# Performance work log

Measured on AMD Instinct MI355X. Metric: run time of the kernel, lower is better.

## Reference

```python
import jax, jax.numpy as jnp
import numpy as np

D_MODEL = 512
N_HEADS = 8
D_KV = 64
EPS = 1e-6
ROPE_THETA = 10000.0


def _rms_norm(x, w):
    # T5-style RMSNorm: no mean subtraction, no bias, variance in fp32.
    var = jnp.mean(x.astype(jnp.float32) ** 2, axis=-1, keepdims=True)
    return (x * jax.lax.rsqrt(var + EPS)).astype(x.dtype) * w


def _rope_cos_sin(pos, dk):
    # pos: [B, T] int -> cos/sin: [B, 1, T, dk]
    inv_freq = 1.0 / (ROPE_THETA ** (jnp.arange(0, dk, 2, dtype=jnp.float32) / dk))
    ang = pos.astype(jnp.float32)[:, :, None] * inv_freq[None, None, :]  # [B,T,dk/2]
    ang = jnp.concatenate([ang, ang], axis=-1)                            # [B,T,dk]
    return jnp.cos(ang)[:, None], jnp.sin(ang)[:, None]


def _rotate_half(x):
    h = x.shape[-1] // 2
    return jnp.concatenate([-x[..., h:], x[..., :h]], axis=-1)


def _mha(x, mask, wq, wk, wv, wo, pos=None):
    # x: [B, T, D]; mask: [B, H, T, T] additive
    B, T, _ = x.shape
    def proj(w):
        return (x @ w).reshape(B, T, N_HEADS, D_KV).transpose(0, 2, 1, 3)  # [B,H,T,dk]
    q, k, v = proj(wq), proj(wk), proj(wv)
    if pos is not None:
        cos, sin = _rope_cos_sin(pos, D_KV)
        cos, sin = cos.astype(x.dtype), sin.astype(x.dtype)
        q = q * cos + _rotate_half(q) * sin
        k = k * cos + _rotate_half(k) * sin
    scale = 1.0 / np.sqrt(D_KV)
    scores = jnp.einsum('bhqd,bhkd->bhqk', q, k) * scale + mask
    attn = jax.nn.softmax(scores.astype(jnp.float32), axis=-1).astype(scores.dtype)
    out = jnp.einsum('bhqk,bhkd->bhqd', attn, v)
    out = out.transpose(0, 2, 1, 3).reshape(B, T, N_HEADS * D_KV)
    return out @ wo


def setup_inputs() -> dict:
    key = jax.random.key(0)
    ks = jax.random.split(key, 12)
    B, T = 8, 1024
    s = 1.0 / np.sqrt(D_MODEL)
    inp = {
        'h': jax.random.normal(ks[0], (B, T, D_MODEL), dtype=jnp.float32),
        'pos': jnp.broadcast_to(jnp.arange(T, dtype=jnp.int64 if jax.config.jax_enable_x64 else jnp.int32)[None, :], (B, T)),
        't_mask': jnp.zeros((B, N_HEADS, T, T), dtype=jnp.float32),
        'g_mask': jnp.zeros((T, N_HEADS, B, B), dtype=jnp.float32),
        'ln_t_w': jnp.ones((D_MODEL,), dtype=jnp.float32),
        'ln_g_w': jnp.ones((D_MODEL,), dtype=jnp.float32),
    }
    names = ['wq_t', 'wk_t', 'wv_t', 'wo_t', 'wq_g', 'wk_g', 'wv_g', 'wo_g']
    for i, n in enumerate(names):
        inp[n] = jax.random.normal(ks[i + 1], (D_MODEL, D_MODEL), dtype=jnp.float32) * s
    return inp


def reference(h, pos, t_mask, g_mask, ln_t_w, ln_g_w,
              wq_t, wk_t, wv_t, wo_t, wq_g, wk_g, wv_g, wo_g):
    # --- time attention (over T axis, with RoPE) ---
    normed = _rms_norm(h, ln_t_w)
    attn_t = _mha(normed, t_mask, wq_t, wk_t, wv_t, wo_t, pos=pos)
    h = h + attn_t  # dropout p=0 (eval)
    # --- group attention (over B axis, no RoPE) ---
    h = h.transpose(1, 0, 2)  # [T, B, D]
    normed = _rms_norm(h, ln_g_w)
    attn_g = _mha(normed, g_mask, wq_g, wk_g, wv_g, wo_g, pos=None)
    h = h + attn_g
    return h.transpose(1, 0, 2)  # back to [B, T, D]
```

## Files before the change

### kernel.cpp

```cpp
#include <hip/hip_runtime.h>
#include <hip/hip_bf16.h>
#include <math.h>


typedef __bf16 bf16x8 __attribute__((ext_vector_type(8)));
typedef __bf16 bf16x4 __attribute__((ext_vector_type(4)));
typedef float  f32x4  __attribute__((ext_vector_type(4)));

#define LN1E4_OVER_32 0.2878231366242558f

__device__ __forceinline__ void gld16(const void* g, void* l) {
    __builtin_amdgcn_global_load_lds((const __attribute__((address_space(1))) void*)g,
                                     (__attribute__((address_space(3))) void*)l,
                                     16, 0, 0);
}

__device__ __forceinline__ int swz64(int r, int c) {
    return r * 64 + (((c + r) & 7) << 3);
}

__global__ __launch_bounds__(256) void prep_k(
    const float* __restrict__ x, const float* __restrict__ wln, __bf16* __restrict__ y,
    const float* w0, const float* w1, const float* w2, const float* w3,
    const float* w4, const float* w5, const float* w6, const float* w7,
    __bf16* qkvT_t, __bf16* oT_t, __bf16* qkvT_g, __bf16* oT_g)
{
    __shared__ float tile[32][33];
    int bid = blockIdx.x;
    if (bid < 2048) {
        int row = bid * 4 + (threadIdx.x >> 6);
        int l = threadIdx.x & 63;
        const float* xr = x + (size_t)row * 512 + l * 8;
        float4 a = *(const float4*)xr;
        float4 b = *(const float4*)(xr + 4);
        float ss = a.x*a.x + a.y*a.y + a.z*a.z + a.w*a.w
                 + b.x*b.x + b.y*b.y + b.z*b.z + b.w*b.w;
        for (int m = 1; m < 64; m <<= 1) ss += __shfl_xor(ss, m);
        float rms = rsqrtf(ss * (1.0f / 512.0f) + 1e-6f);
        float4 wa = *(const float4*)(wln + l * 8);
        float4 wb = *(const float4*)(wln + l * 8 + 4);
        bf16x8 o;
        o[0] = (__bf16)(a.x * rms * wa.x); o[1] = (__bf16)(a.y * rms * wa.y);
        o[2] = (__bf16)(a.z * rms * wa.z); o[3] = (__bf16)(a.w * rms * wa.w);
        o[4] = (__bf16)(b.x * rms * wb.x); o[5] = (__bf16)(b.y * rms * wb.y);
        o[6] = (__bf16)(b.z * rms * wb.z); o[7] = (__bf16)(b.w * rms * wb.w);
        *(bf16x8*)(y + (size_t)row * 512 + l * 8) = o;
        return;
    }
    int bid2 = bid - 2048;
    int mat = bid2 >> 8, rem = bid2 & 255;
    const float* src; __bf16* dst; int rowOff;
    switch (mat) {
        case 0: src=w0; dst=qkvT_t; rowOff=0;    break;
        case 1: src=w1; dst=qkvT_t; rowOff=512;  break;
        case 2: src=w2; dst=qkvT_t; rowOff=1024; break;
        case 3: src=w3; dst=oT_t;   rowOff=0;    break;
        case 4: src=w4; dst=qkvT_g; rowOff=0;    break;
        case 5: src=w5; dst=qkvT_g; rowOff=512;  break;
        case 6: src=w6; dst=qkvT_g; rowOff=1024; break;
        default: src=w7; dst=oT_g;  rowOff=0;    break;
    }
    int n0 = (rem & 15) * 32, k0 = (rem >> 4) * 32;
    int tt = threadIdx.x;
    int kr = tt >> 3, nc = (tt & 7) * 4;
    float4 v = *(const float4*)(src + (size_t)(k0 + kr) * 512 + n0 + nc);
    tile[kr][nc+0] = v.x; tile[kr][nc+1] = v.y; tile[kr][nc+2] = v.z; tile[kr][nc+3] = v.w;
    __syncthreads();
    int nr = tt >> 3, kc = (tt & 7) * 4;
    bf16x4 o;
    o[0] = (__bf16)tile[kc+0][nr]; o[1] = (__bf16)tile[kc+1][nr];
    o[2] = (__bf16)tile[kc+2][nr]; o[3] = (__bf16)tile[kc+3][nr];
    *(bf16x4*)(dst + (size_t)(rowOff + n0 + nr) * 512 + k0 + kc) = o;
}

__global__ __launch_bounds__(256) void rmsnorm_k(
    const float* __restrict__ x, const float* __restrict__ w, __bf16* __restrict__ y)
{
    int row = blockIdx.x * 4 + (threadIdx.x >> 6);
    int l = threadIdx.x & 63;
    const float* xr = x + (size_t)row * 512 + l * 8;
    float4 a = *(const float4*)xr;
    float4 b = *(const float4*)(xr + 4);
    float ss = a.x*a.x + a.y*a.y + a.z*a.z + a.w*a.w
             + b.x*b.x + b.y*b.y + b.z*b.z + b.w*b.w;
    for (int m = 1; m < 64; m <<= 1) ss += __shfl_xor(ss, m);
    float rms = rsqrtf(ss * (1.0f / 512.0f) + 1e-6f);
    float4 wa = *(const float4*)(w + l * 8);
    float4 wb = *(const float4*)(w + l * 8 + 4);
    int orow = (row & 1023) * 8 + (row >> 10);
    bf16x8 o;
    o[0] = (__bf16)(a.x * rms * wa.x); o[1] = (__bf16)(a.y * rms * wa.y);
    o[2] = (__bf16)(a.z * rms * wa.z); o[3] = (__bf16)(a.w * rms * wa.w);
    o[4] = (__bf16)(b.x * rms * wb.x); o[5] = (__bf16)(b.y * rms * wb.y);
    o[6] = (__bf16)(b.z * rms * wb.z); o[7] = (__bf16)(b.w * rms * wb.w);
    *(bf16x8*)(y + (size_t)orow * 512 + l * 8) = o;
}

__global__ __launch_bounds__(256) void gemm_ep(
    const __bf16* __restrict__ A, const __bf16* __restrict__ Bt,
    const int* __restrict__ pos,
    __bf16* __restrict__ o0, __bf16* __restrict__ o1, __bf16* __restrict__ o2,
    int mode)
{
    __shared__ __bf16 smem[16384];
    __bf16* As = smem;
    __bf16* Bs = smem + 8192;
    int tid = threadIdx.x;
    int l = tid & 63, w = tid >> 6;
    int l16 = l & 15, quad = l >> 4;
    int wm = w >> 1, wn = w & 1;
    int mblk = blockIdx.x * 128, nblk = blockIdx.y * 128;
    f32x4 acc[4][4] = {};

    for (int k0 = 0; k0 < 512; k0 += 64) {
        __syncthreads();
        #pragma unroll
        for (int i = 0; i < 4; ++i) {
            int idx = i * 256 + tid;
            int row = idx >> 3, cp = idx & 7;
            int cl = (cp - row) & 7;
            gld16(A  + (size_t)(mblk + row) * 512 + k0 + cl * 8, (char*)As + (size_t)idx * 16);
            gld16(Bt + (size_t)(nblk + row) * 512 + k0 + cl * 8, (char*)Bs + (size_t)idx * 16);
        }
        __syncthreads();
        #pragma unroll
        for (int h = 0; h < 2; h++) {
            bf16x8 aF[4], bF[4];
            #pragma unroll
            for (int mt = 0; mt < 4; mt++) aF[mt] = *(bf16x8*)(As + swz64(wm * 64 + mt * 16 + l16, h * 4 + quad));
            #pragma unroll
            for (int nt = 0; nt < 4; nt++) bF[nt] = *(bf16x8*)(Bs + swz64(wn * 64 + nt * 16 + l16, h * 4 + quad));
            #pragma unroll
            for (int mt = 0; mt < 4; mt++)
                #pragma unroll
                for (int nt = 0; nt < 4; nt++)
                    acc[mt][nt] = __builtin_amdgcn_mfma_f32_16x16x32_bf16(aF[mt], bF[nt], acc[mt][nt], 0, 0, 0);
        }
    }
    __syncthreads();

    int colbase = nblk + wn * 64;
    __bf16* bw = smem + w * 1536;
    int rbrow = l >> 3, rbch = (l & 7) * 8;

    int mat = colbase >> 9;
    int hh  = (colbase & 511) >> 6;
    __bf16* dst = (mat == 0) ? o0 : (mat == 1) ? o1 : o2;
    bool isQ = (mat == 0), isV = (mat == 2);
    if (mode == 0 && !isV) {
        float f0 = __expf((float)l16        * -LN1E4_OVER_32);
        float f1 = __expf((float)(16 + l16) * -LN1E4_OVER_32);
        #pragma unroll
        for (int mt = 0; mt < 4; mt++) {
            int grow0 = mblk + wm * 64 + mt * 16;
            int b = grow0 >> 10, t0 = grow0 & 1023;
            int4 p4 = *(const int4*)&pos[grow0 + quad * 4];
            const int pa[4] = {p4.x, p4.y, p4.z, p4.w};
            #pragma unroll
            for (int r = 0; r < 4; r++) {
                float p = (float)pa[r];
                #pragma unroll
                for (int nt = 0; nt < 2; nt++) {
                    int i = nt * 16 + l16;
                    float ang = p * (nt ? f1 : f0);
                    float c, s; __sincosf(ang, &s, &c);
                    float x1 = acc[mt][nt][r], x2 = acc[mt][nt + 2][r];
                    float y1 = x1 * c - x2 * s;
                    float y2 = x2 * c + x1 * s;
                    if (isQ) { y1 *= 0.125f; y2 *= 0.125f; }
                    bw[(quad * 4 + r) * 72 + i]      = (__bf16)y1;
                    bw[(quad * 4 + r) * 72 + i + 32] = (__bf16)y2;
                }
            }
            #pragma unroll
            for (int i = 0; i < 2; ++i) {
                int rr = rbrow + i * 8;
                bf16x8 vv = *(bf16x8*)&bw[rr * 72 + rbch];
                *(bf16x8*)&dst[((size_t)(b * 8 + hh) * 1024 + t0 + rr) * 64 + rbch] = vv;
            }
        }
    } else if (mode == 0) {
        #pragma unroll
        for (int mt = 0; mt < 4; mt++) {
            #pragma unroll
            for (int nt = 0; nt < 4; nt++)
                #pragma unroll
                for (int r = 0; r < 4; r++)
                    bw[(nt * 16 + l16) * 24 + quad * 4 + r] = (__bf16)acc[mt][nt][r];
            int grow0 = mblk + wm * 64 + mt * 16;
            int b = grow0 >> 10, t0 = grow0 & 1023;
            #pragma unroll
            for (int i = 0; i < 2; ++i) {
                int li = i * 64 + l;
                int d = li >> 1, t8 = (li & 1) * 8;
                bf16x8 vv = *(bf16x8*)&bw[d * 24 + t8];
                *(bf16x8*)&dst[((size_t)(b * 8 + hh) * 64 + d) * 1024 + t0 + t8] = vv;
            }
        }
    } else {
        #pragma unroll
        for (int mt = 0; mt < 4; mt++) {
            int grow0 = mblk + wm * 64 + mt * 16;
            #pragma unroll
            for (int nt = 0; nt < 4; nt++)
                #pragma unroll
                for (int r = 0; r < 4; r++) {
                    float v = acc[mt][nt][r];
                    if (isQ) v *= 0.125f;
                    bw[(quad * 4 + r) * 72 + nt * 16 + l16] = (__bf16)v;
                }
            #pragma unroll
            for (int i = 0; i < 2; ++i) {
                int rr = rbrow + i * 8;
                int grow = grow0 + rr;
                int t = grow >> 3, bq = grow & 7;
                bf16x8 vv = *(bf16x8*)&bw[rr * 72 + rbch];
                *(bf16x8*)&dst[(((size_t)t * 8 + hh) * 8 + bq) * 64 + rbch] = vv;
            }
        }
    }
}

__global__ __launch_bounds__(256) void gemm_o(
    const __bf16* __restrict__ A, const __bf16* __restrict__ Bt,
    const float* __restrict__ resid, float* __restrict__ outF, int remap)
{
    __shared__ __align__(16) char smemraw[24576];
    __bf16* As = (__bf16*)smemraw;
    __bf16* Bs = (__bf16*)(smemraw + 8192);
    int tid = threadIdx.x;
    int l = tid & 63, w = tid >> 6;
    int l16 = l & 15, quad = l >> 4;
    int mblk = blockIdx.x * 64, nblk = blockIdx.y * 128;
    f32x4 acc[8] = {};

    for (int k0 = 0; k0 < 512; k0 += 64) {
        __syncthreads();
        #pragma unroll
        for (int i = 0; i < 2; ++i) {
            int idx = i * 256 + tid;
            int row = idx >> 3, cp = idx & 7;
            int cl = (cp - row) & 7;
            gld16(A + (size_t)(mblk + row) * 512 + k0 + cl * 8, (char*)As + (size_t)idx * 16);
        }
        #pragma unroll
        for (int i = 0; i < 4; ++i) {
            int idx = i * 256 + tid;
            int row = idx >> 3, cp = idx & 7;
            int cl = (cp - row) & 7;
            gld16(Bt + (size_t)(nblk + row) * 512 + k0 + cl * 8, (char*)Bs + (size_t)idx * 16);
        }
        __syncthreads();
        #pragma unroll
        for (int h = 0; h < 2; h++) {
            bf16x8 aF = *(bf16x8*)(As + swz64(w * 16 + l16, h * 4 + quad));
            #pragma unroll
            for (int nt = 0; nt < 8; nt++) {
                bf16x8 bF = *(bf16x8*)(Bs + swz64(nt * 16 + l16, h * 4 + quad));
                acc[nt] = __builtin_amdgcn_mfma_f32_16x16x32_bf16(aF, bF, acc[nt], 0, 0, 0);
            }
        }
    }
    __syncthreads();

    float* fw = (float*)(smemraw + w * 4352);
    int grow0 = mblk + w * 16;
    #pragma unroll
    for (int nh = 0; nh < 2; nh++) {
        #pragma unroll
        for (int nt = 0; nt < 4; nt++)
            #pragma unroll
            for (int r = 0; r < 4; r++)
                fw[(quad * 4 + r) * 68 + nt * 16 + l16] = acc[nh * 4 + nt][r];
        #pragma unroll
        for (int i = 0; i < 4; ++i) {
            int rr = i * 4 + (l >> 4);
            int c4 = (l & 15) * 4;
            f32x4 a4 = *(f32x4*)&fw[rr * 68 + c4];
            int grow = grow0 + rr;
            int orow = remap ? (((grow & 7) << 10) + (grow >> 3)) : grow;
            size_t oi = (size_t)orow * 512 + nblk + nh * 64 + c4;
            f32x4 r4 = *(const f32x4*)&resid[oi];
            r4 += a4;
            *(f32x4*)&outF[oi] = r4;
        }
    }
}

__global__ __launch_bounds__(512) void flash_t(
    const __bf16* __restrict__ q, const __bf16* __restrict__ k,
    const __bf16* __restrict__ vt, const float* __restrict__ tmask,
    __bf16* __restrict__ ctx)
{
    int bh = blockIdx.x;
    int w = threadIdx.x >> 6, l = threadIdx.x & 63;
    int l16 = l & 15, quad = l >> 4;
    int q0 = blockIdx.y * 128 + w * 16;

    __shared__ __bf16 Ks[64 * 72];
    __shared__ __bf16 Vs[64 * 72];
    __shared__ __bf16 Ps[8][16 * 72];

    bf16x8 aQ0, aQ1;
    {
        const __bf16* qp = q + ((size_t)bh * 1024 + q0 + l16) * 64 + quad * 8;
        aQ0 = *(const bf16x8*)qp;
        aQ1 = *(const bf16x8*)(qp + 32);
    }
    f32x4 o[4] = {};
    float l_acc[4] = {0.0f, 0.0f, 0.0f, 0.0f};

    const float* mrow = tmask + (size_t)bh * 1024 * 1024 + (size_t)(q0 + quad * 4) * 1024 + l16;
    float mc[16];
    #pragma unroll
    for (int r = 0; r < 4; r++)
        #pragma unroll
        for (int nt = 0; nt < 4; nt++)
            mc[r * 4 + nt] = __builtin_nontemporal_load(mrow + (size_t)r * 1024 + nt * 16);

    for (int jb = 0; jb < 1024; jb += 64) {
        __syncthreads();
        {
            int c = threadIdx.x;
            int row = c >> 3, col = (c & 7) << 3;
            *(bf16x8*)&Ks[row * 72 + col] = *(const bf16x8*)&k [((size_t)bh * 1024 + jb + row) * 64 + col];
            *(bf16x8*)&Vs[row * 72 + col] = *(const bf16x8*)&vt[((size_t)bh * 64 + row) * 1024 + jb + col];
        }
        __syncthreads();

        float mn_[16];
        {
            int jb2 = (jb + 64) & 1023;
            const float* mr2 = mrow + jb2;
            #pragma unroll
            for (int r = 0; r < 4; r++)
                #pragma unroll
                for (int nt = 0; nt < 4; nt++)
                    mn_[r * 4 + nt] = __builtin_nontemporal_load(mr2 + (size_t)r * 1024 + nt * 16);
        }

        f32x4 s[4] = {};
        #pragma unroll
        for (int nt = 0; nt < 4; nt++) {
            bf16x8 b0 = *(bf16x8*)&Ks[(nt * 16 + l16) * 72 + quad * 8];
            bf16x8 b1 = *(bf16x8*)&Ks[(nt * 16 + l16) * 72 + 32 + quad * 8];
            s[nt] = __builtin_amdgcn_mfma_f32_16x16x32_bf16(aQ0, b0, s[nt], 0, 0, 0);
            s[nt] = __builtin_amdgcn_mfma_f32_16x16x32_bf16(aQ1, b1, s[nt], 0, 0, 0);
        }
        #pragma unroll
        for (int r = 0; r < 4; r++)
            #pragma unroll
            for (int nt = 0; nt < 4; nt++) {
                float p = __expf(s[nt][r] + mc[r * 4 + nt]);
                s[nt][r] = p;
                l_acc[r] += p;
            }

        __bf16* ps = Ps[w];
        #pragma unroll
        for (int nt = 0; nt < 4; nt++)
            #pragma unroll
            for (int r = 0; r < 4; r++)
                ps[(quad * 4 + r) * 72 + nt * 16 + l16] = (__bf16)s[nt][r];
        bf16x8 aP0 = *(bf16x8*)&ps[l16 * 72 + quad * 8];
        bf16x8 aP1 = *(bf16x8*)&ps[l16 * 72 + 32 + quad * 8];
        #pragma unroll
        for (int dt = 0; dt < 4; dt++) {
            bf16x8 bv0 = *(bf16x8*)&Vs[(dt * 16 + l16) * 72 + quad * 8];
            bf16x8 bv1 = *(bf16x8*)&Vs[(dt * 16 + l16) * 72 + 32 + quad * 8];
            o[dt] = __builtin_amdgcn_mfma_f32_16x16x32_bf16(aP0, bv0, o[dt], 0, 0, 0);
            o[dt] = __builtin_amdgcn_mfma_f32_16x16x32_bf16(aP1, bv1, o[dt], 0, 0, 0);
        }

        #pragma unroll
        for (int i = 0; i < 16; i++) mc[i] = mn_[i];
    }

    float l_i[4];
    #pragma unroll
    for (int r = 0; r < 4; r++) {
        float rs = l_acc[r];
        rs += __shfl_xor(rs, 1);
        rs += __shfl_xor(rs, 2);
        rs += __shfl_xor(rs, 4);
        rs += __shfl_xor(rs, 8);
        l_i[r] = rs;
    }

    int b = bh >> 3, h = bh & 7;
    __bf16* ps = Ps[w];
    #pragma unroll
    for (int dt = 0; dt < 4; dt++)
        #pragma unroll
        for (int r = 0; r < 4; r++)
            ps[(quad * 4 + r) * 72 + dt * 16 + l16] = (__bf16)(o[dt][r] / l_i[r]);
    int rbrow = l >> 3, rbch = (l & 7) * 8;
    #pragma unroll
    for (int i = 0; i < 2; ++i) {
        int rr = rbrow + i * 8;
        bf16x8 vv = *(bf16x8*)&ps[rr * 72 + rbch];
        *(bf16x8*)&ctx[((size_t)b * 1024 + q0 + rr) * 512 + h * 64 + rbch] = vv;
    }
}

__global__ __launch_bounds__(256) void group_attn(
    const __bf16* __restrict__ qg, const __bf16* __restrict__ kg,
    const __bf16* __restrict__ vg, const float* __restrict__ gmask,
    __bf16* __restrict__ ctxg)
{
    int tid = blockIdx.x * 256 + threadIdx.x;
    int t = tid >> 6, h = (tid >> 3) & 7, bq = tid & 7;
    size_t base = ((size_t)t * 8 + h) * 512;

    float qv[64];
    #pragma unroll
    for (int d0 = 0; d0 < 64; d0 += 8) {
        bf16x8 qq = *(const bf16x8*)&qg[base + (size_t)bq * 64 + d0];
        #pragma unroll
        for (int u = 0; u < 8; u++) qv[d0 + u] = (float)qq[u];
    }
    float s[8];
    #pragma unroll
    for (int j = 0; j < 8; j++) {
        float acc = 0.0f;
        #pragma unroll
        for (int d0 = 0; d0 < 64; d0 += 8) {
            bf16x8 kk = *(const bf16x8*)&kg[base + (size_t)j * 64 + d0];
            #pragma unroll
            for (int u = 0; u < 8; u++) acc += qv[d0 + u] * (float)kk[u];
        }
        s[j] = acc + gmask[(((size_t)t * 8 + h) * 8 + bq) * 8 + j];
    }
    float mx = s[0];
    #pragma unroll
    for (int j = 1; j < 8; j++) mx = fmaxf(mx, s[j]);
    float sum = 0.0f;
    #pragma unroll
    for (int j = 0; j < 8; j++) { s[j] = __expf(s[j] - mx); sum += s[j]; }
    float inv = 1.0f / sum;

    #pragma unroll
    for (int d0 = 0; d0 < 64; d0 += 8) {
        float o8[8] = {};
        #pragma unroll
        for (int j = 0; j < 8; j++) {
            bf16x8 vv = *(const bf16x8*)&vg[base + (size_t)j * 64 + d0];
            float pj = s[j];
            #pragma unroll
            for (int u = 0; u < 8; u++) o8[u] += pj * (float)vv[u];
        }
        bf16x8 ob;
        #pragma unroll
        for (int u = 0; u < 8; u++) ob[u] = (__bf16)(o8[u] * inv);
        *(bf16x8*)&ctxg[((size_t)t * 8 + bq) * 512 + h * 64 + d0] = ob;
    }
}

extern "C" void kernel_launch(void* const* d_in, const int* in_sizes, int n_in,
                              void* d_out, int out_size, void* d_ws, size_t ws_size,
                              hipStream_t stream)
{
    const float* h      = (const float*)d_in[0];
    const int*   pos    = (const int*)  d_in[1];
    const float* t_mask = (const float*)d_in[2];
    const float* g_mask = (const float*)d_in[3];
    const float* ln_t_w = (const float*)d_in[4];
    const float* ln_g_w = (const float*)d_in[5];
    const float* wq_t = (const float*)d_in[6];
    const float* wk_t = (const float*)d_in[7];
    const float* wv_t = (const float*)d_in[8];
    const float* wo_t = (const float*)d_in[9];
    const float* wq_g = (const float*)d_in[10];
    const float* wk_g = (const float*)d_in[11];
    const float* wv_g = (const float*)d_in[12];
    const float* wo_g = (const float*)d_in[13];
    float* out = (float*)d_out;

    char* ws = (char*)d_ws;
    const size_t MB = 1ull << 20;
    __bf16* qkvT_t = (__bf16*)ws;
    __bf16* oT_t   = qkvT_t + 786432;
    __bf16* qkvT_g = qkvT_t + 1048576;
    __bf16* oT_g   = qkvT_t + 1835008;
    __bf16* normed = (__bf16*)(ws + 4 * MB);
    __bf16* qb     = (__bf16*)(ws + 12 * MB);
    __bf16* kb     = (__bf16*)(ws + 20 * MB);
    __bf16* vb     = (__bf16*)(ws + 28 * MB);
    __bf16* ctx    = (__bf16*)(ws + 36 * MB);
    float*  h2     = (float*) (ws + 44 * MB);

    prep_k<<<4096, 256, 0, stream>>>(h, ln_t_w, normed,
        wq_t, wk_t, wv_t, wo_t, wq_g, wk_g, wv_g, wo_g,
        qkvT_t, oT_t, qkvT_g, oT_g);
    gemm_ep<<<dim3(64, 12), 256, 0, stream>>>(normed, qkvT_t, pos, qb, kb, vb, 0);
    flash_t<<<dim3(64, 8), 512, 0, stream>>>(qb, kb, vb, t_mask, ctx);
    gemm_o<<<dim3(128, 4), 256, 0, stream>>>(ctx, oT_t, h, h2, 0);

    rmsnorm_k<<<2048, 256, 0, stream>>>(h2, ln_g_w, normed);
    gemm_ep<<<dim3(64, 12), 256, 0, stream>>>(normed, qkvT_g, nullptr, qb, kb, vb, 2);
    group_attn<<<256, 256, 0, stream>>>(qb, kb, vb, g_mask, ctx);
    gemm_o<<<dim3(128, 4), 256, 0, stream>>>(ctx, oT_g, h2, out, 1);
}
```

Before: 502.7 us.

## Fuse group RMSNorm into output GEMM epilogue and QKV GEMM row scaling

Removes the standalone rmsnorm kernel for the group branch. The time-attention output GEMM now also writes a transposed bf16 copy of the residual sum and atomically accumulates per-row sums of squares. The group QKV GEMM applies the rsqrt row scale in its epilogue, with the norm weight folded into the weight matrices during prep. This saves a kernel launch and a full read/write pass over the activations, at the cost of atomics, an extra bf16 store in gemm_o, and slightly different rounding because the norm is applied after the matmul.

```diff
diff --git a/kernel.cpp b/kernel.cpp
--- a/kernel.cpp
+++ b/kernel.cpp
@@ -23,11 +23,13 @@
     const float* __restrict__ x, const float* __restrict__ wln, __bf16* __restrict__ y,
     const float* w0, const float* w1, const float* w2, const float* w3,
     const float* w4, const float* w5, const float* w6, const float* w7,
+    const float* __restrict__ gln, float* __restrict__ rmsbuf,
     __bf16* qkvT_t, __bf16* oT_t, __bf16* qkvT_g, __bf16* oT_g)
 {
     __shared__ float tile[32][33];
     int bid = blockIdx.x;
     if (bid < 2048) {
+        if (bid < 32) rmsbuf[bid * 256 + threadIdx.x] = 0.0f;
         int row = bid * 4 + (threadIdx.x >> 6);
         int l = threadIdx.x & 63;
         const float* xr = x + (size_t)row * 512 + l * 8;
@@ -60,6 +62,7 @@
         case 6: src=w6; dst=qkvT_g; rowOff=1024; break;
         default: src=w7; dst=oT_g;  rowOff=0;    break;
     }
+    bool foldG = (mat >= 4 && mat <= 6);
     int n0 = (rem & 15) * 32, k0 = (rem >> 4) * 32;
     int tt = threadIdx.x;
     int kr = tt >> 3, nc = (tt & 7) * 4;
@@ -67,38 +70,20 @@
     tile[kr][nc+0] = v.x; tile[kr][nc+1] = v.y; tile[kr][nc+2] = v.z; tile[kr][nc+3] = v.w;
     __syncthreads();
     int nr = tt >> 3, kc = (tt & 7) * 4;
+    float g0 = 1.f, g1 = 1.f, g2 = 1.f, g3 = 1.f;
+    if (foldG) {
+        float4 gv = *(const float4*)(gln + k0 + kc);
+        g0 = gv.x; g1 = gv.y; g2 = gv.z; g3 = gv.w;
+    }
     bf16x4 o;
-    o[0] = (__bf16)tile[kc+0][nr]; o[1] = (__bf16)tile[kc+1][nr];
-    o[2] = (__bf16)tile[kc+2][nr]; o[3] = (__bf16)tile[kc+3][nr];
+    o[0] = (__bf16)(tile[kc+0][nr] * g0); o[1] = (__bf16)(tile[kc+1][nr] * g1);
+    o[2] = (__bf16)(tile[kc+2][nr] * g2); o[3] = (__bf16)(tile[kc+3][nr] * g3);
     *(bf16x4*)(dst + (size_t)(rowOff + n0 + nr) * 512 + k0 + kc) = o;
-}
-
-__global__ __launch_bounds__(256) void rmsnorm_k(
-    const float* __restrict__ x, const float* __restrict__ w, __bf16* __restrict__ y)
-{
-    int row = blockIdx.x * 4 + (threadIdx.x >> 6);
-    int l = threadIdx.x & 63;
-    const float* xr = x + (size_t)row * 512 + l * 8;
-    float4 a = *(const float4*)xr;
-    float4 b = *(const float4*)(xr + 4);
-    float ss = a.x*a.x + a.y*a.y + a.z*a.z + a.w*a.w
-             + b.x*b.x + b.y*b.y + b.z*b.z + b.w*b.w;
-    for (int m = 1; m < 64; m <<= 1) ss += __shfl_xor(ss, m);
-    float rms = rsqrtf(ss * (1.0f / 512.0f) + 1e-6f);
-    float4 wa = *(const float4*)(w + l * 8);
-    float4 wb = *(const float4*)(w + l * 8 + 4);
-    int orow = (row & 1023) * 8 + (row >> 10);
-    bf16x8 o;
-    o[0] = (__bf16)(a.x * rms * wa.x); o[1] = (__bf16)(a.y * rms * wa.y);
-    o[2] = (__bf16)(a.z * rms * wa.z); o[3] = (__bf16)(a.w * rms * wa.w);
-    o[4] = (__bf16)(b.x * rms * wb.x); o[5] = (__bf16)(b.y * rms * wb.y);
-    o[6] = (__bf16)(b.z * rms * wb.z); o[7] = (__bf16)(b.w * rms * wb.w);
-    *(bf16x8*)(y + (size_t)orow * 512 + l * 8) = o;
 }
 
 __global__ __launch_bounds__(256) void gemm_ep(
     const __bf16* __restrict__ A, const __bf16* __restrict__ Bt,
-    const int* __restrict__ pos,
+    const int* __restrict__ pos, const float* __restrict__ rmsv,
     __bf16* __restrict__ o0, __bf16* __restrict__ o1, __bf16* __restrict__ o2,
     int mode)
 {
@@ -201,14 +186,16 @@
         #pragma unroll
         for (int mt = 0; mt < 4; mt++) {
             int grow0 = mblk + wm * 64 + mt * 16;
+            f32x4 ss4 = *(const f32x4*)&rmsv[grow0 + quad * 4];
+            float rsq[4];
+            #pragma unroll
+            for (int r = 0; r < 4; r++)
+                rsq[r] = rsqrtf(ss4[r] * (1.0f / 512.0f) + 1e-6f) * (isQ ? 0.125f : 1.0f);
             #pragma unroll
             for (int nt = 0; nt < 4; nt++)
                 #pragma unroll
-                for (int r = 0; r < 4; r++) {
-                    float v = acc[mt][nt][r];
-                    if (isQ) v *= 0.125f;
-                    bw[(quad * 4 + r) * 72 + nt * 16 + l16] = (__bf16)v;
-                }
+                for (int r = 0; r < 4; r++)
+                    bw[(quad * 4 + r) * 72 + nt * 16 + l16] = (__bf16)(acc[mt][nt][r] * rsq[r]);
             #pragma unroll
             for (int i = 0; i < 2; ++i) {
                 int rr = rbrow + i * 8;
@@ -223,7 +210,8 @@
 
 __global__ __launch_bounds__(256) void gemm_o(
     const __bf16* __restrict__ A, const __bf16* __restrict__ Bt,
-    const float* __restrict__ resid, float* __restrict__ outF, int remap)
+    const float* __restrict__ resid, float* __restrict__ outF,
+    __bf16* __restrict__ h2b, float* __restrict__ rmsbuf, int remap)
 {
     __shared__ __align__(16) char smemraw[24576];
     __bf16* As = (__bf16*)smemraw;
@@ -265,6 +253,7 @@
 
     float* fw = (float*)(smemraw + w * 4352);
     int grow0 = mblk + w * 16;
+    float ssq[4] = {0.f, 0.f, 0.f, 0.f};
     #pragma unroll
     for (int nh = 0; nh < 2; nh++) {
         #pragma unroll
@@ -283,6 +272,30 @@
             f32x4 r4 = *(const f32x4*)&resid[oi];
             r4 += a4;
             *(f32x4*)&outF[oi] = r4;
+            if (!remap) {
+                int b = grow >> 10, t = grow & 1023;
+                int orow2 = t * 8 + b;
+                bf16x4 h4;
+                h4[0] = (__bf16)r4[0]; h4[1] = (__bf16)r4[1];
+                h4[2] = (__bf16)r4[2]; h4[3] = (__bf16)r4[3];
+                *(bf16x4*)&h2b[(size_t)orow2 * 512 + nblk + nh * 64 + c4] = h4;
+                ssq[i] += r4[0]*r4[0] + r4[1]*r4[1] + r4[2]*r4[2] + r4[3]*r4[3];
+            }
+        }
+    }
+    if (!remap) {
+        #pragma unroll
+        for (int i = 0; i < 4; ++i) {
+            float s = ssq[i];
+            s += __shfl_xor(s, 1);
+            s += __shfl_xor(s, 2);
+            s += __shfl_xor(s, 4);
+            s += __shfl_xor(s, 8);
+            if ((l & 15) == 0) {
+                int grow = grow0 + i * 4 + (l >> 4);
+                int orow2 = (grow & 1023) * 8 + (grow >> 10);
+                atomicAdd(&rmsbuf[orow2], s);
+            }
         }
     }
 }
@@ -488,16 +501,17 @@
     __bf16* vb     = (__bf16*)(ws + 28 * MB);
     __bf16* ctx    = (__bf16*)(ws + 36 * MB);
     float*  h2     = (float*) (ws + 44 * MB);
+    float*  rmsbuf = (float*) (ws + 60 * MB);
+    __bf16* h2b    = (__bf16*)(ws + 61 * MB);
 
     prep_k<<<4096, 256, 0, stream>>>(h, ln_t_w, normed,
         wq_t, wk_t, wv_t, wo_t, wq_g, wk_g, wv_g, wo_g,
-        qkvT_t, oT_t, qkvT_g, oT_g);
-    gemm_ep<<<dim3(64, 12), 256, 0, stream>>>(normed, qkvT_t, pos, qb, kb, vb, 0);
+        ln_g_w, rmsbuf, qkvT_t, oT_t, qkvT_g, oT_g);
+    gemm_ep<<<dim3(64, 12), 256, 0, stream>>>(normed, qkvT_t, pos, nullptr, qb, kb, vb, 0);
     flash_t<<<dim3(64, 8), 512, 0, stream>>>(qb, kb, vb, t_mask, ctx);
-    gemm_o<<<dim3(128, 4), 256, 0, stream>>>(ctx, oT_t, h, h2, 0);
-
-    rmsnorm_k<<<2048, 256, 0, stream>>>(h2, ln_g_w, normed);
-    gemm_ep<<<dim3(64, 12), 256, 0, stream>>>(normed, qkvT_g, nullptr, qb, kb, vb, 2);
+    gemm_o<<<dim3(128, 4), 256, 0, stream>>>(ctx, oT_t, h, h2, h2b, rmsbuf, 0);
+
+    gemm_ep<<<dim3(64, 12), 256, 0, stream>>>(h2b, qkvT_g, nullptr, rmsbuf, qb, kb, vb, 2);
     group_attn<<<256, 256, 0, stream>>>(qb, kb, vb, g_mask, ctx);
-    gemm_o<<<dim3(128, 4), 256, 0, stream>>>(ctx, oT_g, h2, out, 1);
-}
+    gemm_o<<<dim3(128, 4), 256, 0, stream>>>(ctx, oT_g, h2, out, nullptr, nullptr, 1);
+}
```

Result: no change. 499.2 us (-0.7%).
